# Kernel optimization log

Hardware: AMD Instinct MI355X
Metric: run time of the kernel (lower is better)

## Reference

```python
import jax, jax.numpy as jnp
import numpy as np

EMBED = 768
HEADS = 12


def setup_inputs() -> dict:
    key = jax.random.key(0)
    k1, k2, k3 = jax.random.split(key, 3)
    B, N, E = 2, 2048, EMBED
    x = jax.random.normal(k1, (B, N, E), dtype=jnp.float32)
    w_qkv = jax.random.normal(k2, (3 * E, E), dtype=jnp.float32) * (1.0 / np.sqrt(E))
    b_qkv = jnp.zeros((3 * E,), dtype=jnp.float32)
    w_o = jax.random.normal(k3, (E, E), dtype=jnp.float32) * (1.0 / np.sqrt(E))
    b_o = jnp.zeros((E,), dtype=jnp.float32)
    return {"x": x, "w_qkv": w_qkv, "b_qkv": b_qkv, "w_o": w_o, "b_o": b_o}


def reference(x, w_qkv, b_qkv, w_o, b_o):
    B, N, E = x.shape
    H = HEADS
    d = E // H
    # fused qkv projection (torch Linear: x @ W^T + b)
    qkv = x @ w_qkv.T + b_qkv                       # [B, N, 3E]
    # Rearrange 'b n (h qkv e) -> b qkv h n e'
    qkv = qkv.reshape(B, N, H, 3, d).transpose(0, 3, 2, 1, 4)  # [B, 3, H, N, d]
    q, k, v = qkv[:, 0], qkv[:, 1], qkv[:, 2]       # each [B, H, N, d]
    scores = jnp.einsum("bhqd,bhkd->bhqk", q, k)    # [B, H, N, N]
    attn = jax.nn.softmax(scores / jnp.sqrt(jnp.float32(E)), axis=-1)
    ctx = jnp.einsum("bhqk,bhkd->bhqd", attn, v)    # [B, H, N, d]
    ctx = ctx.transpose(0, 2, 1, 3).reshape(B, N, E)  # 'b h n d -> b n (h d)'
    out = ctx @ w_o.T + b_o
    return out
```

## Files before the change

### kernel.cpp

```cpp
#include <hip/hip_runtime.h>

#define BB 2
#define NN 2048
#define EE 768
#define HH 12
#define DD 64
#define MM (BB*NN)
#define E3 (3*EE)
#define QSCALE 0.05205877280961602f

typedef __bf16 bf16x8 __attribute__((ext_vector_type(8)));
typedef float  f32x4  __attribute__((ext_vector_type(4)));
typedef unsigned short u16x8 __attribute__((ext_vector_type(8)));

#define MFMA(a,b,c) __builtin_amdgcn_mfma_f32_16x16x32_bf16(a,b,c,0,0,0)

__device__ __forceinline__ unsigned short f2bf(float f) {
    unsigned int u = __float_as_uint(f);
    u += 0x7FFFu + ((u >> 16) & 1u);
    return (unsigned short)(u >> 16);
}

typedef __attribute__((address_space(3))) unsigned int as3u32;
typedef __attribute__((address_space(1))) unsigned int as1u32;
__device__ __forceinline__ void gll16(const void* g, void* l) {
    __builtin_amdgcn_global_load_lds((const as1u32*)(uintptr_t)g,
                                     (as3u32*)(unsigned int)(uintptr_t)l, 16, 0, 0);
}

#define XB4 786432
#define WQ4 442368
#define WO4 147456
__global__ __launch_bounds__(256)
void cast3(const float* __restrict__ x, const float* __restrict__ wq,
           const float* __restrict__ wo, unsigned short* __restrict__ dst) {
    int i = blockIdx.x * 256 + threadIdx.x;
    const float* src;
    int off;
    if (i < XB4)            { src = x;  off = i; }
    else if (i < XB4+WQ4)   { src = wq; off = i - XB4; }
    else                    { src = wo; off = i - XB4 - WQ4; }
    float4 v = ((const float4*)src)[off];
    ushort4 o;
    o.x = f2bf(v.x); o.y = f2bf(v.y); o.z = f2bf(v.z); o.w = f2bf(v.w);
    ((ushort4*)dst)[i] = o;
}

__global__ __launch_bounds__(256)
void gemm_qkv(const unsigned short* __restrict__ A, const unsigned short* __restrict__ W,
              const float* __restrict__ bias,
              unsigned short* __restrict__ o0, unsigned short* __restrict__ o1,
              unsigned short* __restrict__ o2)
{
    __shared__ unsigned short As[128 * 32];
    __shared__ unsigned short Bs[128 * 32];

    const int tid = threadIdx.x;
    const int l = tid & 63;
    const int w = tid >> 6;
    const int m0 = blockIdx.x * 128;
    const int c0 = blockIdx.y * 128;
    const int wm = (w >> 1) * 64;
    const int wn = (w & 1) * 64;

    const int s0 = w * 2;
    const unsigned short* a_src0 = A + (size_t)(m0 + s0*16      + (l>>2)) * EE + (l&3)*8;
    const unsigned short* a_src1 = A + (size_t)(m0 + (s0+1)*16  + (l>>2)) * EE + (l&3)*8;
    const unsigned short* b_src0 = W + (size_t)(c0 + s0*16      + (l>>2)) * EE + (l&3)*8;
    const unsigned short* b_src1 = W + (size_t)(c0 + (s0+1)*16  + (l>>2)) * EE + (l&3)*8;
    unsigned short* a_dst0 = &As[s0*512];
    unsigned short* a_dst1 = &As[(s0+1)*512];
    unsigned short* b_dst0 = &Bs[s0*512];
    unsigned short* b_dst1 = &Bs[(s0+1)*512];

    const f32x4 zero4 = {0.f, 0.f, 0.f, 0.f};
    f32x4 acc[4][4];
    #pragma unroll
    for (int i = 0; i < 4; ++i)
        #pragma unroll
        for (int j = 0; j < 4; ++j) acc[i][j] = zero4;

    for (int k0 = 0; k0 < EE; k0 += 32) {
        __syncthreads();
        gll16(a_src0 + k0, a_dst0);
        gll16(a_src1 + k0, a_dst1);
        gll16(b_src0 + k0, b_dst0);
        gll16(b_src1 + k0, b_dst1);
        __syncthreads();

        bf16x8 af[4], bf[4];
        #pragma unroll
        for (int i = 0; i < 4; ++i)
            af[i] = *(const bf16x8*)&As[(wm + 16*i + (l&15))*32 + (l>>4)*8];
        #pragma unroll
        for (int j = 0; j < 4; ++j)
            bf[j] = *(const bf16x8*)&Bs[(wn + 16*j + (l&15))*32 + (l>>4)*8];
        #pragma unroll
        for (int i = 0; i < 4; ++i)
            #pragma unroll
            for (int j = 0; j < 4; ++j)
                acc[i][j] = MFMA(af[i], bf[j], acc[i][j]);
    }

    const int sec = (c0 + wn) >> 6;
    const int hh = sec / 3;
    const int tt = sec - hh*3;
    #pragma unroll
    for (int j = 0; j < 4; ++j) {
        const int col = c0 + wn + 16*j + (l&15);
        const int dcol = 16*j + (l&15);
        const float bj = bias[col];
        #pragma unroll
        for (int i = 0; i < 4; ++i) {
            const int row0 = m0 + wm + 16*i + (l>>4)*4;
            const int b = row0 >> 11;
            const int n = row0 & (NN - 1);
            if (tt == 2) {
                ushort4 pk;
                pk.x = f2bf(acc[i][j][0] + bj);
                pk.y = f2bf(acc[i][j][1] + bj);
                pk.z = f2bf(acc[i][j][2] + bj);
                pk.w = f2bf(acc[i][j][3] + bj);
                *(ushort4*)&o2[(((size_t)b*HH + hh)*DD + dcol)*NN + n] = pk;
            } else {
                unsigned short* dst = (tt == 0) ? o0 : o1;
                #pragma unroll
                for (int r = 0; r < 4; ++r) {
                    float val = acc[i][j][r] + bj;
                    if (tt == 0) val *= QSCALE;
                    dst[(((size_t)b*HH + hh)*NN + n + r)*DD + dcol] = f2bf(val);
                }
            }
        }
    }
}

__global__ __launch_bounds__(256)
void gemm_out(const unsigned short* __restrict__ A, const unsigned short* __restrict__ W,
              const float* __restrict__ bias, float* __restrict__ of)
{
    __shared__ unsigned short As[64 * 32];
    __shared__ unsigned short Bs[128 * 32];

    const int tid = threadIdx.x;
    const int l = tid & 63;
    const int w = tid >> 6;
    const int m0 = blockIdx.x * 64;
    const int c0 = blockIdx.y * 128;
    const int wm = (w >> 1) * 32;
    const int wn = (w & 1) * 64;

    const unsigned short* s_src[3];
    unsigned short* s_dst[3];
    #pragma unroll
    for (int s = 0; s < 3; ++s) {
        const int ch = 3*w + s;
        if (ch < 4) {
            s_src[s] = A + (size_t)(m0 + ch*16 + (l>>2)) * EE + (l&3)*8;
            s_dst[s] = &As[ch*512];
        } else {
            s_src[s] = W + (size_t)(c0 + (ch-4)*16 + (l>>2)) * EE + (l&3)*8;
            s_dst[s] = &Bs[(ch-4)*512];
        }
    }

    const f32x4 zero4 = {0.f, 0.f, 0.f, 0.f};
    f32x4 acc[2][4];
    #pragma unroll
    for (int i = 0; i < 2; ++i)
        #pragma unroll
        for (int j = 0; j < 4; ++j) acc[i][j] = zero4;

    for (int k0 = 0; k0 < EE; k0 += 32) {
        __syncthreads();
        #pragma unroll
        for (int s = 0; s < 3; ++s) gll16(s_src[s] + k0, s_dst[s]);
        __syncthreads();

        bf16x8 af[2], bf[4];
        #pragma unroll
        for (int i = 0; i < 2; ++i)
            af[i] = *(const bf16x8*)&As[(wm + 16*i + (l&15))*32 + (l>>4)*8];
        #pragma unroll
        for (int j = 0; j < 4; ++j)
            bf[j] = *(const bf16x8*)&Bs[(wn + 16*j + (l&15))*32 + (l>>4)*8];
        #pragma unroll
        for (int i = 0; i < 2; ++i)
            #pragma unroll
            for (int j = 0; j < 4; ++j)
                acc[i][j] = MFMA(af[i], bf[j], acc[i][j]);
    }

    #pragma unroll
    for (int j = 0; j < 4; ++j) {
        const int col = c0 + wn + 16*j + (l&15);
        const float bj = bias[col];
        #pragma unroll
        for (int i = 0; i < 2; ++i) {
            #pragma unroll
            for (int r = 0; r < 4; ++r) {
                const int row = m0 + wm + 16*i + (l>>4)*4 + r;
                of[(size_t)row * EE + col] = acc[i][j][r] + bj;
            }
        }
    }
}

__global__ __launch_bounds__(256)
void attn_mfma(const unsigned short* __restrict__ Q, const unsigned short* __restrict__ K,
               const unsigned short* __restrict__ Vt_g, unsigned short* __restrict__ ctx)
{
    __shared__ unsigned short Ks[64 * 64];
    __shared__ unsigned short Vt[64 * 64];
    __shared__ unsigned short Pq[4 * 16 * 64];

    const int tid = threadIdx.x;
    const int l = tid & 63;
    const int w = tid >> 6;
    const int quad = l >> 4;
    const int lc = l & 15;
    const int x7 = lc & 7;

    const int id = blockIdx.x;
    const int bh = id % 24;
    const int bq = id / 24;
    const int b  = bh / 12;
    const int h  = bh - b*12;
    const size_t hb = (size_t)bh * NN * DD;

    const f32x4 zero4 = {0.f, 0.f, 0.f, 0.f};

    const int qrow = bq*64 + w*16 + lc;
    const bf16x8 qf0 = *(const bf16x8*)(Q + hb + (size_t)qrow*DD +      quad*8);
    const bf16x8 qf1 = *(const bf16x8*)(Q + hb + (size_t)qrow*DD + 32 + quad*8);

    f32x4 o[4];
    #pragma unroll
    for (int dj = 0; dj < 4; ++dj) o[dj] = zero4;
    float lsum = 0.f;

    const int srow = tid >> 2;
    const int sc = tid & 3;
    const unsigned short* kbase = K + hb + (size_t)srow*DD + sc*16;
    const unsigned short* vbase = Vt_g + ((size_t)bh*DD + srow)*NN + sc*16;
    const int c0s = ((2*sc)     ^ (srow & 7)) * 8;
    const int c1s = ((2*sc + 1) ^ (srow & 7)) * 8;
    unsigned short* ksl0 = &Ks[srow*64 + c0s];
    unsigned short* ksl1 = &Ks[srow*64 + c1s];
    unsigned short* vsl0 = &Vt[srow*64 + c0s];
    unsigned short* vsl1 = &Vt[srow*64 + c1s];

    const int chq0 = ((    quad) ^ x7) * 8;
    const int chq1 = ((4 + quad) ^ x7) * 8;
    const int pw = w * 1024;
    const int prd0 = pw + lc*64 + (((      2*quad) ^ (lc & 14)) * 4);
    const int prd1 = pw + lc*64 + (((8 +   2*quad) ^ (lc & 14)) * 4);

    for (int kt = 0; kt < NN/64; ++kt) {
        const unsigned short* ksrc = kbase + (size_t)kt*64*DD;
        const unsigned short* vsrc = vbase + kt*64;
        u16x8 k0 = *(const u16x8*)ksrc;
        u16x8 k1 = *(const u16x8*)(ksrc + 8);
        u16x8 v0 = *(const u16x8*)vsrc;
        u16x8 v1 = *(const u16x8*)(vsrc + 8);
        __syncthreads();
        *(u16x8*)ksl0 = k0;
        *(u16x8*)ksl1 = k1;
        *(u16x8*)vsl0 = v0;
        *(u16x8*)vsl1 = v1;
        __syncthreads();

        f32x4 st[4];
        #pragma unroll
        for (int jf = 0; jf < 4; ++jf) {
            bf16x8 kf0 = *(const bf16x8*)&Ks[(16*jf + lc)*64 + chq0];
            bf16x8 kf1 = *(const bf16x8*)&Ks[(16*jf + lc)*64 + chq1];
            f32x4 acc0 = MFMA(kf0, qf0, zero4);
            st[jf] = MFMA(kf1, qf1, acc0);
        }

        #pragma unroll
        for (int jf = 0; jf < 4; ++jf) {
            float e0 = __builtin_amdgcn_exp2f(st[jf][0]);
            float e1 = __builtin_amdgcn_exp2f(st[jf][1]);
            float e2 = __builtin_amdgcn_exp2f(st[jf][2]);
            float e3 = __builtin_amdgcn_exp2f(st[jf][3]);
            lsum += (e0 + e1) + (e2 + e3);
            ushort4 pk;
            pk.x = f2bf(e0); pk.y = f2bf(e1); pk.z = f2bf(e2); pk.w = f2bf(e3);
            *(ushort4*)&Pq[pw + lc*64 + (((4*jf + quad) ^ (lc & 14)) * 4)] = pk;
        }

        {
            bf16x8 pf0 = *(const bf16x8*)&Pq[prd0];
            bf16x8 pf1 = *(const bf16x8*)&Pq[prd1];
            #pragma unroll
            for (int dj = 0; dj < 4; ++dj) {
                bf16x8 vf0 = *(const bf16x8*)&Vt[(16*dj + lc)*64 + chq0];
                bf16x8 vf1 = *(const bf16x8*)&Vt[(16*dj + lc)*64 + chq1];
                o[dj] = MFMA(vf0, pf0, o[dj]);
                o[dj] = MFMA(vf1, pf1, o[dj]);
            }
        }
    }

    lsum += __shfl_xor(lsum, 16);
    lsum += __shfl_xor(lsum, 32);
    const float inv = 1.f / lsum;

    const int n = bq*64 + w*16 + lc;
    #pragma unroll
    for (int dj = 0; dj < 4; ++dj) {
        ushort4 pk;
        pk.x = f2bf(o[dj][0] * inv);
        pk.y = f2bf(o[dj][1] * inv);
        pk.z = f2bf(o[dj][2] * inv);
        pk.w = f2bf(o[dj][3] * inv);
        *(ushort4*)&ctx[((size_t)(b*NN + n))*EE + h*DD + 16*dj + quad*4] = pk;
    }
}

extern "C" void kernel_launch(void* const* d_in, const int* in_sizes, int n_in,
                              void* d_out, int out_size, void* d_ws, size_t ws_size,
                              hipStream_t stream)
{
    const float* x     = (const float*)d_in[0];
    const float* w_qkv = (const float*)d_in[1];
    const float* b_qkv = (const float*)d_in[2];
    const float* w_o   = (const float*)d_in[3];
    const float* b_o   = (const float*)d_in[4];
    float* out = (float*)d_out;

    unsigned short* wsu = (unsigned short*)d_ws;
    const size_t XB = (size_t)MM * EE;
    const size_t WQ = (size_t)E3 * EE;
    const size_t WO = (size_t)EE * EE;
    const size_t HS = (size_t)BB * HH * NN * DD;
    unsigned short* xb   = wsu;
    unsigned short* wqb  = xb  + XB;
    unsigned short* wob  = wqb + WQ;
    unsigned short* qb   = wob + WO;
    unsigned short* kb   = qb  + HS;
    unsigned short* vtb  = kb  + HS;
    unsigned short* ctxb = vtb + HS;

    cast3<<<(XB4 + WQ4 + WO4)/256, 256, 0, stream>>>(x, w_qkv, w_o, xb);

    dim3 g1(MM/128, E3/128);
    gemm_qkv<<<g1, 256, 0, stream>>>(xb, wqb, b_qkv, qb, kb, vtb);

    attn_mfma<<<768, 256, 0, stream>>>(qb, kb, vtb, ctxb);

    dim3 g3(MM/64, EE/128);
    gemm_out<<<g3, 256, 0, stream>>>(ctxb, wob, b_o, out);
}
```

Before: 173.6 us.

## Prefetch next K/V tile into registers and store Q transposed

The attention loop now loads the next K/V tile from global memory into registers right after the shared-memory store, so the load latency overlaps the current tile's MFMA and softmax work instead of stalling before the barrier. Separately, the QKV GEMM writes Q in the same transposed [d][n] layout as V, using packed 4-element stores instead of scalar strided stores, and the attention kernel gathers Q fragments with strided scalar loads once per block. This trades cheaper GEMM epilogue writes for a slower one-time Q load, and holds the prefetched tile in extra registers.

```diff
diff --git a/kernel.cpp b/kernel.cpp
--- a/kernel.cpp
+++ b/kernel.cpp
@@ -115,20 +115,20 @@
             const int row0 = m0 + wm + 16*i + (l>>4)*4;
             const int b = row0 >> 11;
             const int n = row0 & (NN - 1);
-            if (tt == 2) {
+            if (tt != 1) {
+                unsigned short* dst = (tt == 0) ? o0 : o2;
+                const float scl = (tt == 0) ? QSCALE : 1.f;
                 ushort4 pk;
-                pk.x = f2bf(acc[i][j][0] + bj);
-                pk.y = f2bf(acc[i][j][1] + bj);
-                pk.z = f2bf(acc[i][j][2] + bj);
-                pk.w = f2bf(acc[i][j][3] + bj);
-                *(ushort4*)&o2[(((size_t)b*HH + hh)*DD + dcol)*NN + n] = pk;
+                pk.x = f2bf((acc[i][j][0] + bj) * scl);
+                pk.y = f2bf((acc[i][j][1] + bj) * scl);
+                pk.z = f2bf((acc[i][j][2] + bj) * scl);
+                pk.w = f2bf((acc[i][j][3] + bj) * scl);
+                *(ushort4*)&dst[(((size_t)b*HH + hh)*DD + dcol)*NN + n] = pk;
             } else {
-                unsigned short* dst = (tt == 0) ? o0 : o1;
                 #pragma unroll
                 for (int r = 0; r < 4; ++r) {
-                    float val = acc[i][j][r] + bj;
-                    if (tt == 0) val *= QSCALE;
-                    dst[(((size_t)b*HH + hh)*NN + n + r)*DD + dcol] = f2bf(val);
+                    o1[(((size_t)b*HH + hh)*NN + n + r)*DD + dcol] =
+                        f2bf(acc[i][j][r] + bj);
                 }
             }
         }
@@ -207,7 +207,7 @@
 }
 
 __global__ __launch_bounds__(256)
-void attn_mfma(const unsigned short* __restrict__ Q, const unsigned short* __restrict__ K,
+void attn_mfma(const unsigned short* __restrict__ Qt_g, const unsigned short* __restrict__ K,
                const unsigned short* __restrict__ Vt_g, unsigned short* __restrict__ ctx)
 {
     __shared__ unsigned short Ks[64 * 64];
@@ -231,8 +231,14 @@
     const f32x4 zero4 = {0.f, 0.f, 0.f, 0.f};
 
     const int qrow = bq*64 + w*16 + lc;
-    const bf16x8 qf0 = *(const bf16x8*)(Q + hb + (size_t)qrow*DD +      quad*8);
-    const bf16x8 qf1 = *(const bf16x8*)(Q + hb + (size_t)qrow*DD + 32 + quad*8);
+    u16x8 q0r, q1r;
+    #pragma unroll
+    for (int j = 0; j < 8; ++j) {
+        q0r[j] = Qt_g[hb + (size_t)(     quad*8 + j)*NN + qrow];
+        q1r[j] = Qt_g[hb + (size_t)(32 + quad*8 + j)*NN + qrow];
+    }
+    const bf16x8 qf0 = __builtin_bit_cast(bf16x8, q0r);
+    const bf16x8 qf1 = __builtin_bit_cast(bf16x8, q1r);
 
     f32x4 o[4];
     #pragma unroll
@@ -242,33 +248,44 @@
     const int srow = tid >> 2;
     const int sc = tid & 3;
     const unsigned short* kbase = K + hb + (size_t)srow*DD + sc*16;
-    const unsigned short* vbase = Vt_g + ((size_t)bh*DD + srow)*NN + sc*16;
+    const unsigned short* vbase = Vt_g + hb + (size_t)srow*NN + sc*16;
     const int c0s = ((2*sc)     ^ (srow & 7)) * 8;
     const int c1s = ((2*sc + 1) ^ (srow & 7)) * 8;
-    unsigned short* ksl0 = &Ks[srow*64 + c0s];
-    unsigned short* ksl1 = &Ks[srow*64 + c1s];
-    unsigned short* vsl0 = &Vt[srow*64 + c0s];
-    unsigned short* vsl1 = &Vt[srow*64 + c1s];
+    const int so = srow * 64;
 
     const int chq0 = ((    quad) ^ x7) * 8;
     const int chq1 = ((4 + quad) ^ x7) * 8;
     const int pw = w * 1024;
-    const int prd0 = pw + lc*64 + (((      2*quad) ^ (lc & 14)) * 4);
-    const int prd1 = pw + lc*64 + (((8 +   2*quad) ^ (lc & 14)) * 4);
+    const int prd0 = pw + lc*64 + (((    2*quad) ^ (lc & 14)) * 4);
+    const int prd1 = pw + lc*64 + (((8 + 2*quad) ^ (lc & 14)) * 4);
+
+    u16x8 rk0, rk1, rv0, rv1;
+    {
+        const unsigned short* kp = kbase;
+        const unsigned short* vp = vbase;
+        rk0 = *(const u16x8*)kp;
+        rk1 = *(const u16x8*)(kp + 8);
+        rv0 = *(const u16x8*)vp;
+        rv1 = *(const u16x8*)(vp + 8);
+    }
 
     for (int kt = 0; kt < NN/64; ++kt) {
-        const unsigned short* ksrc = kbase + (size_t)kt*64*DD;
-        const unsigned short* vsrc = vbase + kt*64;
-        u16x8 k0 = *(const u16x8*)ksrc;
-        u16x8 k1 = *(const u16x8*)(ksrc + 8);
-        u16x8 v0 = *(const u16x8*)vsrc;
-        u16x8 v1 = *(const u16x8*)(vsrc + 8);
-        __syncthreads();
-        *(u16x8*)ksl0 = k0;
-        *(u16x8*)ksl1 = k1;
-        *(u16x8*)vsl0 = v0;
-        *(u16x8*)vsl1 = v1;
-        __syncthreads();
+        __syncthreads();
+        *(u16x8*)&Ks[so + c0s] = rk0;
+        *(u16x8*)&Ks[so + c1s] = rk1;
+        *(u16x8*)&Vt[so + c0s] = rv0;
+        *(u16x8*)&Vt[so + c1s] = rv1;
+        __syncthreads();
+
+        {
+            const int ktn = (kt + 1 < NN/64) ? kt + 1 : kt;
+            const unsigned short* kp = kbase + (size_t)ktn*64*DD;
+            const unsigned short* vp = vbase + ktn*64;
+            rk0 = *(const u16x8*)kp;
+            rk1 = *(const u16x8*)(kp + 8);
+            rv0 = *(const u16x8*)vp;
+            rv1 = *(const u16x8*)(vp + 8);
+        }
 
         f32x4 st[4];
         #pragma unroll
@@ -339,17 +356,17 @@
     unsigned short* xb   = wsu;
     unsigned short* wqb  = xb  + XB;
     unsigned short* wob  = wqb + WQ;
-    unsigned short* qb   = wob + WO;
-    unsigned short* kb   = qb  + HS;
+    unsigned short* qtb  = wob + WO;
+    unsigned short* kb   = qtb + HS;
     unsigned short* vtb  = kb  + HS;
     unsigned short* ctxb = vtb + HS;
 
     cast3<<<(XB4 + WQ4 + WO4)/256, 256, 0, stream>>>(x, w_qkv, w_o, xb);
 
     dim3 g1(MM/128, E3/128);
-    gemm_qkv<<<g1, 256, 0, stream>>>(xb, wqb, b_qkv, qb, kb, vtb);
-
-    attn_mfma<<<768, 256, 0, stream>>>(qb, kb, vtb, ctxb);
+    gemm_qkv<<<g1, 256, 0, stream>>>(xb, wqb, b_qkv, qtb, kb, vtb);
+
+    attn_mfma<<<768, 256, 0, stream>>>(qtb, kb, vtb, ctxb);
 
     dim3 g3(MM/64, EE/128);
     gemm_out<<<g3, 256, 0, stream>>>(ctxb, wob, b_o, out);
```

Measured after the change: 175.7 us. Within noise of the previous version (+1.2%).

## Split attention keys across waves and keep K, V and P in registers

Applied to the files above, without the earlier changes.

The attention kernel now gives each wave a slice of 16 keys per tile for all 64 queries, instead of 16 queries against all keys. K and V fragments are loaded straight from global memory into registers, with the next K tile prefetched, so the per-tile LDS staging and both block barriers are gone. The P fragment is packed in registers and fed to a 16x16x16 MFMA. At the end the four waves' partial outputs and row sums are combined through shared memory. This removes LDS traffic and synchronisation from the inner loop, but adds a cross-wave reduction, more accumulator registers (launch bounds set to 3 blocks per CU) and uncoalesced small V loads.

```diff
diff --git a/kernel.cpp b/kernel.cpp
--- a/kernel.cpp
+++ b/kernel.cpp
@@ -12,8 +12,12 @@
 typedef __bf16 bf16x8 __attribute__((ext_vector_type(8)));
 typedef float  f32x4  __attribute__((ext_vector_type(4)));
 typedef unsigned short u16x8 __attribute__((ext_vector_type(8)));
-
-#define MFMA(a,b,c) __builtin_amdgcn_mfma_f32_16x16x32_bf16(a,b,c,0,0,0)
+typedef unsigned short u16x4 __attribute__((ext_vector_type(4)));
+typedef short s16x4 __attribute__((ext_vector_type(4)));
+typedef unsigned int u32x2 __attribute__((ext_vector_type(2)));
+
+#define MFMA(a,b,c)   __builtin_amdgcn_mfma_f32_16x16x32_bf16(a,b,c,0,0,0)
+#define MFMA16(a,b,c) __builtin_amdgcn_mfma_f32_16x16x16bf16_1k(a,b,c,0,0,0)
 
 __device__ __forceinline__ unsigned short f2bf(float f) {
     unsigned int u = __float_as_uint(f);
@@ -206,20 +210,20 @@
     }
 }
 
-__global__ __launch_bounds__(256)
-void attn_mfma(const unsigned short* __restrict__ Q, const unsigned short* __restrict__ K,
+__global__ __launch_bounds__(256, 3)
+void attn_mfma(const unsigned short* __restrict__ Qg, const unsigned short* __restrict__ K,
                const unsigned short* __restrict__ Vt_g, unsigned short* __restrict__ ctx)
 {
-    __shared__ unsigned short Ks[64 * 64];
-    __shared__ unsigned short Vt[64 * 64];
-    __shared__ unsigned short Pq[4 * 16 * 64];
+    __shared__ unsigned char smem[35840];
+    unsigned short* Qs = (unsigned short*)smem;
+    float* Red = (float*)smem;
+    float* Ls  = (float*)(smem + 34816);
 
     const int tid = threadIdx.x;
     const int l = tid & 63;
     const int w = tid >> 6;
     const int quad = l >> 4;
     const int lc = l & 15;
-    const int x7 = lc & 7;
 
     const int id = blockIdx.x;
     const int bh = id % 24;
@@ -230,93 +234,143 @@
 
     const f32x4 zero4 = {0.f, 0.f, 0.f, 0.f};
 
-    const int qrow = bq*64 + w*16 + lc;
-    const bf16x8 qf0 = *(const bf16x8*)(Q + hb + (size_t)qrow*DD +      quad*8);
-    const bf16x8 qf1 = *(const bf16x8*)(Q + hb + (size_t)qrow*DD + 32 + quad*8);
-
-    f32x4 o[4];
-    #pragma unroll
-    for (int dj = 0; dj < 4; ++dj) o[dj] = zero4;
-    float lsum = 0.f;
-
-    const int srow = tid >> 2;
-    const int sc = tid & 3;
-    const unsigned short* kbase = K + hb + (size_t)srow*DD + sc*16;
-    const unsigned short* vbase = Vt_g + ((size_t)bh*DD + srow)*NN + sc*16;
-    const int c0s = ((2*sc)     ^ (srow & 7)) * 8;
-    const int c1s = ((2*sc + 1) ^ (srow & 7)) * 8;
-    unsigned short* ksl0 = &Ks[srow*64 + c0s];
-    unsigned short* ksl1 = &Ks[srow*64 + c1s];
-    unsigned short* vsl0 = &Vt[srow*64 + c0s];
-    unsigned short* vsl1 = &Vt[srow*64 + c1s];
-
-    const int chq0 = ((    quad) ^ x7) * 8;
-    const int chq1 = ((4 + quad) ^ x7) * 8;
-    const int pw = w * 1024;
-    const int prd0 = pw + lc*64 + (((      2*quad) ^ (lc & 14)) * 4);
-    const int prd1 = pw + lc*64 + (((8 +   2*quad) ^ (lc & 14)) * 4);
-
-    for (int kt = 0; kt < NN/64; ++kt) {
-        const unsigned short* ksrc = kbase + (size_t)kt*64*DD;
-        const unsigned short* vsrc = vbase + kt*64;
-        u16x8 k0 = *(const u16x8*)ksrc;
-        u16x8 k1 = *(const u16x8*)(ksrc + 8);
-        u16x8 v0 = *(const u16x8*)vsrc;
-        u16x8 v1 = *(const u16x8*)(vsrc + 8);
-        __syncthreads();
-        *(u16x8*)ksl0 = k0;
-        *(u16x8*)ksl1 = k1;
-        *(u16x8*)vsl0 = v0;
-        *(u16x8*)vsl1 = v1;
-        __syncthreads();
-
+    {
+        const int row = tid >> 2;
+        const int col = (tid & 3) * 16;
+        const unsigned short* src = Qg + hb + (size_t)(bq*64 + row)*DD + col;
+        u16x8 qa = *(const u16x8*)src;
+        u16x8 qb2 = *(const u16x8*)(src + 8);
+        *(u16x8*)&Qs[row*64 + col]     = qa;
+        *(u16x8*)&Qs[row*64 + col + 8] = qb2;
+    }
+    __syncthreads();
+    bf16x8 qf[4][2];
+    #pragma unroll
+    for (int g = 0; g < 4; ++g)
+        #pragma unroll
+        for (int ks = 0; ks < 2; ++ks)
+            qf[g][ks] = *(const bf16x8*)&Qs[(g*16 + lc)*64 + ks*32 + quad*8];
+
+    f32x4 O[4][4];
+    #pragma unroll
+    for (int db = 0; db < 4; ++db)
+        #pragma unroll
+        for (int g = 0; g < 4; ++g) O[db][g] = zero4;
+    float lsum[4] = {0.f, 0.f, 0.f, 0.f};
+
+    const unsigned short* kp = K + hb + (size_t)(w*16 + lc)*DD + quad*8;
+    const unsigned short* vp[4];
+    #pragma unroll
+    for (int db = 0; db < 4; ++db)
+        vp[db] = Vt_g + hb + (size_t)(db*16 + lc)*NN + w*16 + quad*4;
+
+    u16x8 rk0 = *(const u16x8*)kp;
+    u16x8 rk1 = *(const u16x8*)(kp + 32);
+    kp += 64*DD;
+
+    for (int t = 0; t < NN/64; ++t) {
+        u16x4 rv[4];
+        #pragma unroll
+        for (int db = 0; db < 4; ++db) {
+            rv[db] = *(const u16x4*)vp[db];
+            vp[db] += 64;
+        }
+
+        bf16x8 kf0 = __builtin_bit_cast(bf16x8, rk0);
+        bf16x8 kf1 = __builtin_bit_cast(bf16x8, rk1);
         f32x4 st[4];
         #pragma unroll
-        for (int jf = 0; jf < 4; ++jf) {
-            bf16x8 kf0 = *(const bf16x8*)&Ks[(16*jf + lc)*64 + chq0];
-            bf16x8 kf1 = *(const bf16x8*)&Ks[(16*jf + lc)*64 + chq1];
-            f32x4 acc0 = MFMA(kf0, qf0, zero4);
-            st[jf] = MFMA(kf1, qf1, acc0);
-        }
-
-        #pragma unroll
-        for (int jf = 0; jf < 4; ++jf) {
-            float e0 = __builtin_amdgcn_exp2f(st[jf][0]);
-            float e1 = __builtin_amdgcn_exp2f(st[jf][1]);
-            float e2 = __builtin_amdgcn_exp2f(st[jf][2]);
-            float e3 = __builtin_amdgcn_exp2f(st[jf][3]);
-            lsum += (e0 + e1) + (e2 + e3);
-            ushort4 pk;
-            pk.x = f2bf(e0); pk.y = f2bf(e1); pk.z = f2bf(e2); pk.w = f2bf(e3);
-            *(ushort4*)&Pq[pw + lc*64 + (((4*jf + quad) ^ (lc & 14)) * 4)] = pk;
-        }
-
-        {
-            bf16x8 pf0 = *(const bf16x8*)&Pq[prd0];
-            bf16x8 pf1 = *(const bf16x8*)&Pq[prd1];
-            #pragma unroll
-            for (int dj = 0; dj < 4; ++dj) {
-                bf16x8 vf0 = *(const bf16x8*)&Vt[(16*dj + lc)*64 + chq0];
-                bf16x8 vf1 = *(const bf16x8*)&Vt[(16*dj + lc)*64 + chq1];
-                o[dj] = MFMA(vf0, pf0, o[dj]);
-                o[dj] = MFMA(vf1, pf1, o[dj]);
+        for (int g = 0; g < 4; ++g) {
+            f32x4 t0 = MFMA(kf0, qf[g][0], zero4);
+            st[g] = MFMA(kf1, qf[g][1], t0);
+        }
+
+        rk0 = *(const u16x8*)kp;
+        rk1 = *(const u16x8*)(kp + 32);
+        kp += 64*DD;
+
+        s16x4 pf[4];
+        #pragma unroll
+        for (int g = 0; g < 4; ++g) {
+            float e0 = __builtin_amdgcn_exp2f(st[g][0]);
+            float e1 = __builtin_amdgcn_exp2f(st[g][1]);
+            float e2 = __builtin_amdgcn_exp2f(st[g][2]);
+            float e3 = __builtin_amdgcn_exp2f(st[g][3]);
+            lsum[g] += (e0 + e1) + (e2 + e3);
+            unsigned int p01 = __builtin_amdgcn_perm(__float_as_uint(e1) + 0x8000u,
+                                                     __float_as_uint(e0) + 0x8000u, 0x07060302u);
+            unsigned int p23 = __builtin_amdgcn_perm(__float_as_uint(e3) + 0x8000u,
+                                                     __float_as_uint(e2) + 0x8000u, 0x07060302u);
+            u32x2 pp = {p01, p23};
+            pf[g] = __builtin_bit_cast(s16x4, pp);
+        }
+
+        #pragma unroll
+        for (int db = 0; db < 4; ++db) {
+            s16x4 vfr = __builtin_bit_cast(s16x4, rv[db]);
+            #pragma unroll
+            for (int g = 0; g < 4; ++g)
+                O[db][g] = MFMA16(vfr, pf[g], O[db][g]);
+        }
+    }
+
+    #pragma unroll
+    for (int g = 0; g < 4; ++g) {
+        lsum[g] += __shfl_xor(lsum[g], 16);
+        lsum[g] += __shfl_xor(lsum[g], 32);
+    }
+    __syncthreads();
+    if (quad == 0) {
+        #pragma unroll
+        for (int g = 0; g < 4; ++g) Ls[w*64 + g*16 + lc] = lsum[g];
+    }
+    if (w & 1) {
+        float* R = Red + (w >> 1) * 4352;
+        #pragma unroll
+        for (int db = 0; db < 4; ++db)
+            #pragma unroll
+            for (int g = 0; g < 4; ++g)
+                *(f32x4*)&R[(g*16 + lc)*68 + db*16 + quad*4] = O[db][g];
+    }
+    __syncthreads();
+    if (!(w & 1)) {
+        float* R = Red + (w >> 1) * 4352;
+        #pragma unroll
+        for (int db = 0; db < 4; ++db)
+            #pragma unroll
+            for (int g = 0; g < 4; ++g)
+                O[db][g] += *(const f32x4*)&R[(g*16 + lc)*68 + db*16 + quad*4];
+    }
+    __syncthreads();
+    if (w == 2) {
+        #pragma unroll
+        for (int db = 0; db < 4; ++db)
+            #pragma unroll
+            for (int g = 0; g < 4; ++g)
+                *(f32x4*)&Red[(g*16 + lc)*68 + db*16 + quad*4] = O[db][g];
+    }
+    __syncthreads();
+    if (w == 0) {
+        float inv[4];
+        #pragma unroll
+        for (int g = 0; g < 4; ++g) {
+            const int q = g*16 + lc;
+            inv[g] = 1.f / (Ls[q] + Ls[64 + q] + Ls[128 + q] + Ls[192 + q]);
+        }
+        #pragma unroll
+        for (int db = 0; db < 4; ++db) {
+            #pragma unroll
+            for (int g = 0; g < 4; ++g) {
+                f32x4 o = O[db][g] + *(const f32x4*)&Red[(g*16 + lc)*68 + db*16 + quad*4];
+                ushort4 pk;
+                pk.x = f2bf(o[0] * inv[g]);
+                pk.y = f2bf(o[1] * inv[g]);
+                pk.z = f2bf(o[2] * inv[g]);
+                pk.w = f2bf(o[3] * inv[g]);
+                const int n = bq*64 + g*16 + lc;
+                *(ushort4*)&ctx[((size_t)(b*NN + n))*EE + h*DD + db*16 + quad*4] = pk;
             }
         }
-    }
-
-    lsum += __shfl_xor(lsum, 16);
-    lsum += __shfl_xor(lsum, 32);
-    const float inv = 1.f / lsum;
-
-    const int n = bq*64 + w*16 + lc;
-    #pragma unroll
-    for (int dj = 0; dj < 4; ++dj) {
-        ushort4 pk;
-        pk.x = f2bf(o[dj][0] * inv);
-        pk.y = f2bf(o[dj][1] * inv);
-        pk.z = f2bf(o[dj][2] * inv);
-        pk.w = f2bf(o[dj][3] * inv);
-        *(ushort4*)&ctx[((size_t)(b*NN + n))*EE + h*DD + 16*dj + quad*4] = pk;
     }
 }
 
```

Result: slower. 199.6 us (+15.0%).
